# Kernel tuning notes

Measured on AMD Instinct MI355X. Metric: run time of the kernel, lower is better.

The kernel has to match this reference:

```python
import jax, jax.numpy as jnp
import numpy as np

EPS = 1e-5
B, N = 16, 131072

def _bn(x, g, b, m, v):
    # x: [C, N]; inference-mode batchnorm with given stats
    return g[:, None] * (x - m[:, None]) * jax.lax.rsqrt(v[:, None] + EPS) + b[:, None]

def _make_npts():
    base = N // B
    offs = np.linspace(-2048, 2048, B).astype(np.int64)
    npts = np.full(B, base, dtype=np.int64) + offs
    npts[-1] += N - npts.sum()
    assert npts.sum() == N and (npts > 0).all()
    return npts

def setup_inputs() -> dict:
    key = jax.random.key(0)
    ks = jax.random.split(key, 16)
    d = {}
    d["x"] = jax.random.normal(ks[0], (3, N), jnp.float32)
    d["npts"] = jnp.asarray(_make_npts(), jnp.int32)
    def w(k, o, i):
        return jax.random.normal(k, (o, i), jnp.float32) * (1.0 / np.sqrt(i))
    def bnp(k, c):
        k1, k2, k3, k4 = jax.random.split(k, 4)
        return (1.0 + 0.1 * jax.random.normal(k1, (c,), jnp.float32),
                0.1 * jax.random.normal(k2, (c,), jnp.float32),
                0.1 * jax.random.normal(k3, (c,), jnp.float32),
                0.5 + jax.random.uniform(k4, (c,), jnp.float32))
    d["W1"] = w(ks[1], 128, 3);   d["b1"] = jnp.zeros(128, jnp.float32)
    d["g1"], d["be1"], d["m1"], d["v1"] = bnp(ks[2], 128)
    d["W2"] = w(ks[3], 256, 128); d["b2"] = jnp.zeros(256, jnp.float32)
    d["g2"], d["be2"], d["m2"], d["v2"] = bnp(ks[4], 256)
    d["W3"] = w(ks[5], 512, 512); d["b3"] = jnp.zeros(512, jnp.float32)
    d["g3"], d["be3"], d["m3"], d["v3"] = bnp(ks[6], 512)
    d["W4"] = w(ks[7], 1024, 512); d["b4"] = jnp.zeros(1024, jnp.float32)
    d["g4"], d["be4"], d["m4"], d["v4"] = bnp(ks[8], 1024)
    return d

def reference(x, npts,
              W1, b1, g1, be1, m1, v1,
              W2, b2, g2, be2, m2, v2,
              W3, b3, g3, be3, m3, v3,
              W4, b4, g4, be4, m4, v4):
    # segment ids for the ragged point->cloud mapping (replaces torch.split loops)
    seg = jnp.repeat(jnp.arange(B, dtype=jnp.int32), npts, total_repeat_length=N)  # [N]
    h = jax.nn.relu(_bn(W1 @ x + b1[:, None], g1, be1, m1, v1))        # [128, N]
    f = _bn(W2 @ h + b2[:, None], g2, be2, m2, v2)                      # [256, N]
    g = jax.ops.segment_max(f.T, seg, num_segments=B)                   # [B, 256]
    gs = g[seg].T                                                       # [256, N] broadcast back
    xc = jnp.concatenate([gs, f], axis=0)                               # [512, N]
    h3 = jax.nn.relu(_bn(W3 @ xc + b3[:, None], g3, be3, m3, v3))       # [512, N]
    h4 = _bn(W4 @ h3 + b4[:, None], g4, be4, m4, v4)                    # [1024, N]
    v = jax.ops.segment_max(h4.T, seg, num_segments=B)                  # [B, 1024]
    return v
```

## Files before the change

### kernel.cpp

```cpp
#include <hip/hip_runtime.h>
#include <hip/hip_bf16.h>
#include <stdint.h>

#define NTOT 131072
#define NSEG 16
#define EPSV 1e-5f

typedef __attribute__((ext_vector_type(8))) short bf16x8;
typedef __attribute__((ext_vector_type(4))) float f32x4;

struct Args {
  const float* x; const int* npts;
  const float *W1,*b1,*g1,*be1,*m1,*v1;
  const float *W2,*b2,*g2,*be2,*m2,*v2;
  const float *W3,*b3,*g3,*be3,*m3,*v3;
  const float *W4,*b4,*g4,*be4,*m4,*v4;
  int* offs;
  float *a1,*c1,*a2,*c2,*a3,*c3,*a4,*c4;
  unsigned int *gkeys,*vkeys;
  unsigned short *w2b;
  unsigned short *w3p;
  unsigned short *w4p;
  unsigned short *fbufp;
  unsigned short *h3p;
  float* cseg;
  float* out;
};

__device__ inline unsigned int f2key(float f){ unsigned u=__float_as_uint(f); return (u&0x80000000u)? ~u : (u|0x80000000u); }
__device__ inline float key2f(unsigned k){ unsigned u=(k&0x80000000u)? (k^0x80000000u) : ~k; return __uint_as_float(u); }
__device__ inline unsigned short f2bf(float f){ __hip_bfloat16 h=__float2bfloat16(f); return *(unsigned short*)&h; }

__device__ inline void gl16(const void* g, void* l){
  __builtin_amdgcn_global_load_lds((const __attribute__((address_space(1))) unsigned int*)g,
                                   (__attribute__((address_space(3))) unsigned int*)l, 16, 0, 0);
}

__global__ void k_setup(Args A){
  int tid = threadIdx.x;
  if (tid==0){ int s=0; A.offs[0]=0; for (int i=0;i<NSEG;i++){ s+=A.npts[i]; A.offs[i+1]=s; } }
  for (int c=tid;c<128;c+=256){ float a=A.g1[c]*rsqrtf(A.v1[c]+EPSV); A.a1[c]=a; A.c1[c]=A.be1[c]+a*(A.b1[c]-A.m1[c]); }
  for (int c=tid;c<256;c+=256){ float a=A.g2[c]*rsqrtf(A.v2[c]+EPSV); A.a2[c]=a; A.c2[c]=A.be2[c]+a*(A.b2[c]-A.m2[c]); }
  for (int c=tid;c<512;c+=256){ float a=A.g3[c]*rsqrtf(A.v3[c]+EPSV); A.a3[c]=a; A.c3[c]=A.be3[c]+a*(A.b3[c]-A.m3[c]); }
  for (int c=tid;c<1024;c+=256){ float a=A.g4[c]*rsqrtf(A.v4[c]+EPSV); A.a4[c]=a; A.c4[c]=A.be4[c]+a*(A.b4[c]-A.m4[c]); }
  for (int i=tid;i<NSEG*256;i+=256)  A.gkeys[i]=0u;
  for (int i=tid;i<NSEG*1024;i+=256) A.vkeys[i]=0u;
}

__global__ void k_conv(Args A){
  const int n1=256*128;
  const int n2=8*4*512*8;
  const int n3=16*4*1024*8;
  for (int i = blockIdx.x*256+threadIdx.x; i < n1+n2+n3; i += gridDim.x*256){
    if (i<n1) A.w2b[i]=f2bf(A.W2[i]);
    else if (i<n1+n2){
      int o=i-n1; int j=o&7, cout=(o>>3)&511, g=o>>12; int ks=g>>2, kg=g&3;
      A.w3p[o]=f2bf(A.W3[(size_t)cout*512 + 256 + ks*32+kg*8+j]);
    } else {
      int o=i-n1-n2; int j=o&7, cout=(o>>3)&1023, g=o>>13; int ks=g>>2, kg=g&3;
      A.w4p[o]=f2bf(A.W4[(size_t)cout*512 + ks*32+kg*8+j]);
    }
  }
}

__global__ __launch_bounds__(256) void k_l12(Args A){
  __shared__ float w1s[384], a1s[128], c1s[128], a2s[256], c2s[256];
  __shared__ float xs[3][64];
  __shared__ int offs_s[NSEG+1], segp[64];
  __shared__ unsigned short hs[16*64*8];
  int tid=threadIdx.x, pt0=blockIdx.x*64;
  for (int i=tid;i<384;i+=256) w1s[i]=A.W1[i];
  if (tid<128){ a1s[tid]=A.a1[tid]; c1s[tid]=A.c1[tid]; }
  a2s[tid]=A.a2[tid]; c2s[tid]=A.c2[tid];
  if (tid<=NSEG) offs_s[tid]=A.offs[tid];
  if (tid<64){ xs[0][tid]=A.x[pt0+tid]; xs[1][tid]=A.x[NTOT+pt0+tid]; xs[2][tid]=A.x[2*NTOT+pt0+tid]; }
  __syncthreads();
  if (tid<64){ int gp=pt0+tid, s=0; while (gp>=offs_s[s+1]) s++; segp[tid]=s; }
  for (int pair=tid; pair<1024; pair+=256){
    int pt=pair&63, kc=pair>>6;
    float x0=xs[0][pt], x1=xs[1][pt], x2=xs[2][pt];
    unsigned short us[8];
    #pragma unroll
    for (int j=0;j<8;j++){
      int cin=kc*8+j;
      float v = fmaf(w1s[cin*3],x0, fmaf(w1s[cin*3+1],x1, w1s[cin*3+2]*x2));
      v = fmaxf(fmaf(a1s[cin],v,c1s[cin]), 0.f);
      us[j]=f2bf(v);
    }
    uint4 pk;
    pk.x=(unsigned)us[0]|((unsigned)us[1]<<16); pk.y=(unsigned)us[2]|((unsigned)us[3]<<16);
    pk.z=(unsigned)us[4]|((unsigned)us[5]<<16); pk.w=(unsigned)us[6]|((unsigned)us[7]<<16);
    *(uint4*)(&hs[(kc*64+pt)*8]) = pk;
  }
  __syncthreads();
  int lane=tid&63, wv=tid>>6, quad=lane>>4, l16=lane&15;
  int m0=wv*64;
  f32x4 acc[4][4];
  for (int a=0;a<4;a++)
    for (int b=0;b<4;b++)
      acc[a][b]=(f32x4){0.f,0.f,0.f,0.f};
  #pragma unroll
  for (int ks=0; ks<4; ++ks){
    bf16x8 bfr[4];
    #pragma unroll
    for (int nt=0; nt<4; ++nt) bfr[nt]=*(bf16x8*)(&hs[((ks*4+quad)*64 + nt*16 + l16)*8]);
    #pragma unroll
    for (int mt=0; mt<4; ++mt){
      bf16x8 afr = *(const bf16x8*)(&A.w2b[(m0+mt*16+l16)*128 + ks*32 + quad*8]);
      #pragma unroll
      for (int nt=0; nt<4; ++nt)
        acc[mt][nt]=__builtin_amdgcn_mfma_f32_16x16x32_bf16(afr, bfr[nt], acc[mt][nt], 0,0,0);
    }
  }
  bool uni = (segp[0]==segp[63]); int seg0=segp[0];
  size_t tb = (size_t)blockIdx.x*16384;
  #pragma unroll
  for (int mt=0;mt<4;++mt){
    int cout0=m0+mt*16+quad*4;
    int kg=cout0>>3, sub=cout0&7;
    float fv[4][4];
    #pragma unroll
    for (int nt=0;nt<4;++nt)
      #pragma unroll
      for (int r=0;r<4;++r)
        fv[nt][r]=fmaf(a2s[cout0+r], acc[mt][nt][r], c2s[cout0+r]);
    #pragma unroll
    for (int nt=0;nt<4;++nt){
      int ptl=nt*16+l16;
      uint2 pk;
      pk.x=(unsigned)f2bf(fv[nt][0])|((unsigned)f2bf(fv[nt][1])<<16);
      pk.y=(unsigned)f2bf(fv[nt][2])|((unsigned)f2bf(fv[nt][3])<<16);
      *(uint2*)&A.fbufp[tb + (size_t)((kg*64+ptl)*8+sub)] = pk;
    }
    #pragma unroll
    for (int r=0;r<4;++r){
      if (uni){
        float mv=fmaxf(fmaxf(fv[0][r],fv[1][r]),fmaxf(fv[2][r],fv[3][r]));
        #pragma unroll
        for (int off=8;off>=1;off>>=1) mv=fmaxf(mv, __shfl_xor(mv,off));
        if (l16==0) atomicMax(&A.gkeys[seg0*256+cout0+r], f2key(mv));
      } else {
        #pragma unroll
        for (int nt=0;nt<4;++nt)
          atomicMax(&A.gkeys[segp[nt*16+l16]*256+cout0+r], f2key(fv[nt][r]));
      }
    }
  }
}

__global__ void k_cseg(Args A){
  int seg = blockIdx.x>>1; int cout = (blockIdx.x&1)*256 + threadIdx.x;
  __shared__ float gs[256];
  gs[threadIdx.x] = key2f(A.gkeys[seg*256+threadIdx.x]);
  __syncthreads();
  const float* wrow = A.W3 + (size_t)cout*512;
  float s=0.f;
  #pragma unroll 8
  for (int k=0;k<256;k++) s = fmaf(wrow[k], gs[k], s);
  A.cseg[seg*512+cout]=s;
}

__global__ __launch_bounds__(512,2) void k_l3(Args A){
  __shared__ unsigned short wlds[8*4*256*8];
  __shared__ int offs_s[NSEG+1];
  int bid=blockIdx.x; int xcd=bid&7; int j=bid>>3;
  int cgrp=j&1, ptgrp=xcd*64+(j>>1);
  int tid=threadIdx.x, lane=tid&63, wv=tid>>6, quad=lane>>4, l16=lane&15;
  int mq=wv&1, tq=wv>>1;
  for (int i=wv*16;i<wv*16+16;++i){
    int slice=i>>2, q=i&3;
    const char* src=(const char*)(A.w3p + (size_t)slice*4096 + cgrp*2048 + q*512);
    gl16(src + lane*16, (char*)wlds + slice*4096 + q*1024);
  }
  if (tid<=NSEG) offs_s[tid]=A.offs[tid];
  __syncthreads();
  int tg = ptgrp*4 + tq, pt0 = tg*64;
  int sBeg=0; while (pt0 >= offs_s[sBeg+1]) sBeg++;
  int sEnd=sBeg; while (pt0+63 >= offs_s[sEnd+1]) sEnd++;
  bool uni=(sBeg==sEnd);
  int segl[4];
  if (!uni){
    #pragma unroll
    for (int nt=0;nt<4;++nt){ int gp=pt0+nt*16+l16, s=sBeg; while (gp>=offs_s[s+1]) s++; segl[nt]=s; }
  }
  f32x4 acc[8][4];
  for (int a=0;a<8;a++)
    for (int b=0;b<4;b++)
      acc[a][b]=(f32x4){0.f,0.f,0.f,0.f};
  const unsigned short* bsrc = A.fbufp + (size_t)tg*16384;
  bf16x8 bb[2][4];
  #pragma unroll
  for (int nt=0;nt<4;++nt) bb[0][nt]=*(const bf16x8*)(bsrc + (size_t)((quad*64 + nt*16 + l16)*8));
  #pragma unroll
  for (int nt=0;nt<4;++nt) bb[1][nt]=*(const bf16x8*)(bsrc + (size_t)(((4+quad)*64 + nt*16 + l16)*8));
  #pragma unroll
  for (int ksl=0; ksl<8; ++ksl){
    bf16x8 afr[8];
    #pragma unroll
    for (int mt=0;mt<8;++mt) afr[mt]=*(bf16x8*)(&wlds[((ksl*4+quad)*256 + mq*128 + mt*16 + l16)*8]);
    #pragma unroll
    for (int mt=0;mt<8;++mt)
      #pragma unroll
      for (int nt=0;nt<4;++nt)
        acc[mt][nt]=__builtin_amdgcn_mfma_f32_16x16x32_bf16(afr[mt], bb[ksl&1][nt], acc[mt][nt], 0,0,0);
    if (ksl+2<8){
      #pragma unroll
      for (int nt=0;nt<4;++nt) bb[ksl&1][nt]=*(const bf16x8*)(bsrc + (size_t)((((ksl+2)*4+quad)*64 + nt*16 + l16)*8));
    }
  }
  #pragma unroll
  for (int mt=0;mt<8;++mt){
    int cout0=cgrp*256 + mq*128 + mt*16 + quad*4;
    int kg=cout0>>3, sub=cout0&7;
    float sa[4],sc[4],csr[4];
    #pragma unroll
    for (int r=0;r<4;++r){ sa[r]=A.a3[cout0+r]; sc[r]=A.c3[cout0+r]; }
    if (uni){
      #pragma unroll
      for (int r=0;r<4;++r) csr[r]=A.cseg[sBeg*512+cout0+r];
    }
    #pragma unroll
    for (int nt=0;nt<4;++nt){
      int ptl=nt*16+l16;
      unsigned short us[4];
      #pragma unroll
      for (int r=0;r<4;++r){
        float cv = uni? csr[r] : A.cseg[segl[nt]*512+cout0+r];
        float hv = fmaxf(fmaf(sa[r], acc[mt][nt][r]+cv, sc[r]), 0.f);
        us[r]=f2bf(hv);
      }
      uint2 pk;
      pk.x=(unsigned)us[0]|((unsigned)us[1]<<16);
      pk.y=(unsigned)us[2]|((unsigned)us[3]<<16);
      *(uint2*)&A.h3p[(size_t)tg*32768 + (size_t)((kg*64+ptl)*8+sub)] = pk;
    }
  }
}

__global__ __launch_bounds__(512,2) void k_l4(Args A){
  __shared__ unsigned short wlds[16*4*128*8];
  __shared__ int offs_s[NSEG+1];
  int bid=blockIdx.x; int xcd=bid&7; int j=bid>>3;
  int cgrp=j&7, ptgrp=xcd*32+(j>>3);
  int tid=threadIdx.x, lane=tid&63, wv=tid>>6, quad=lane>>4, l16=lane&15;
  for (int i=wv*16;i<wv*16+16;++i){
    int slice=i>>1, half=i&1;
    const char* src=(const char*)(A.w4p + (size_t)slice*8192 + cgrp*1024 + half*512);
    gl16(src + lane*16, (char*)wlds + slice*2048 + half*1024);
  }
  if (tid<=NSEG) offs_s[tid]=A.offs[tid];
  __syncthreads();
  int tg = ptgrp*8 + wv, pt0 = tg*64;
  int sBeg=0; while (pt0 >= offs_s[sBeg+1]) sBeg++;
  int sEnd=sBeg; while (pt0+63 >= offs_s[sEnd+1]) sEnd++;
  bool uni=(sBeg==sEnd);
  int segl[4];
  if (!uni){
    #pragma unroll
    for (int nt=0;nt<4;++nt){ int gp=pt0+nt*16+l16, s=sBeg; while (gp>=offs_s[s+1]) s++; segl[nt]=s; }
  }
  f32x4 acc[8][4];
  for (int a=0;a<8;a++)
    for (int b=0;b<4;b++)
      acc[a][b]=(f32x4){0.f,0.f,0.f,0.f};
  const unsigned short* bsrc = A.h3p + (size_t)tg*32768;
  bf16x8 bb[2][4];
  #pragma unroll
  for (int nt=0;nt<4;++nt) bb[0][nt]=*(const bf16x8*)(bsrc + (size_t)((quad*64 + nt*16 + l16)*8));
  #pragma unroll
  for (int nt=0;nt<4;++nt) bb[1][nt]=*(const bf16x8*)(bsrc + (size_t)(((4+quad)*64 + nt*16 + l16)*8));
  #pragma unroll
  for (int ksl=0; ksl<16; ++ksl){
    bf16x8 afr[8];
    #pragma unroll
    for (int mt=0;mt<8;++mt) afr[mt]=*(bf16x8*)(&wlds[((ksl*4+quad)*128 + mt*16 + l16)*8]);
    #pragma unroll
    for (int mt=0;mt<8;++mt)
      #pragma unroll
      for (int nt=0;nt<4;++nt)
        acc[mt][nt]=__builtin_amdgcn_mfma_f32_16x16x32_bf16(afr[mt], bb[ksl&1][nt], acc[mt][nt], 0,0,0);
    if (ksl+2<16){
      #pragma unroll
      for (int nt=0;nt<4;++nt) bb[ksl&1][nt]=*(const bf16x8*)(bsrc + (size_t)((((ksl+2)*4+quad)*64 + nt*16 + l16)*8));
    }
  }
  #pragma unroll
  for (int mt=0;mt<8;++mt){
    int cout0=cgrp*128 + mt*16 + quad*4;
    #pragma unroll
    for (int r=0;r<4;++r){
      int cout=cout0+r;
      float sa=A.a4[cout], sc=A.c4[cout];
      float mv=-3.4e38f;
      #pragma unroll
      for (int nt=0;nt<4;++nt){
        float fv=fmaf(sa, acc[mt][nt][r], sc);
        if (uni) mv=fmaxf(mv,fv);
        else atomicMax(&A.vkeys[segl[nt]*1024+cout], f2key(fv));
      }
      if (uni){
        #pragma unroll
        for (int off=8;off>=1;off>>=1) mv=fmaxf(mv, __shfl_xor(mv,off));
        if (l16==0) atomicMax(&A.vkeys[sBeg*1024+cout], f2key(mv));
      }
    }
  }
}

__global__ void k_final(Args A){
  int i=blockIdx.x*256+threadIdx.x;
  if (i<NSEG*1024) A.out[i]=key2f(A.vkeys[i]);
}

extern "C" void kernel_launch(void* const* d_in, const int* in_sizes, int n_in,
                              void* d_out, int out_size, void* d_ws, size_t ws_size,
                              hipStream_t stream){
  Args A;
  A.x  =(const float*)d_in[0];  A.npts=(const int*)d_in[1];
  A.W1 =(const float*)d_in[2];  A.b1 =(const float*)d_in[3];
  A.g1 =(const float*)d_in[4];  A.be1=(const float*)d_in[5];
  A.m1 =(const float*)d_in[6];  A.v1 =(const float*)d_in[7];
  A.W2 =(const float*)d_in[8];  A.b2 =(const float*)d_in[9];
  A.g2 =(const float*)d_in[10]; A.be2=(const float*)d_in[11];
  A.m2 =(const float*)d_in[12]; A.v2 =(const float*)d_in[13];
  A.W3 =(const float*)d_in[14]; A.b3 =(const float*)d_in[15];
  A.g3 =(const float*)d_in[16]; A.be3=(const float*)d_in[17];
  A.m3 =(const float*)d_in[18]; A.v3 =(const float*)d_in[19];
  A.W4 =(const float*)d_in[20]; A.b4 =(const float*)d_in[21];
  A.g4 =(const float*)d_in[22]; A.be4=(const float*)d_in[23];
  A.m4 =(const float*)d_in[24]; A.v4 =(const float*)d_in[25];

  char* w=(char*)d_ws;
  auto alloc=[&](size_t b)->void*{ void* p=(void*)w; w += (b+255)&~(size_t)255; return p; };
  A.offs =(int*)alloc((NSEG+1)*4);
  A.a1=(float*)alloc(128*4);  A.c1=(float*)alloc(128*4);
  A.a2=(float*)alloc(256*4);  A.c2=(float*)alloc(256*4);
  A.a3=(float*)alloc(512*4);  A.c3=(float*)alloc(512*4);
  A.a4=(float*)alloc(1024*4); A.c4=(float*)alloc(1024*4);
  A.gkeys=(unsigned int*)alloc(NSEG*256*4);
  A.vkeys=(unsigned int*)alloc(NSEG*1024*4);
  A.cseg =(float*)alloc(NSEG*512*4);
  A.w2b=(unsigned short*)alloc(256*128*2);
  A.w3p=(unsigned short*)alloc(131072*2);
  A.w4p=(unsigned short*)alloc(524288*2);
  A.fbufp=(unsigned short*)alloc((size_t)2048*16384*2);
  A.h3p  =(unsigned short*)alloc((size_t)2048*32768*2);
  A.out=(float*)d_out;

  k_setup<<<dim3(1),dim3(256),0,stream>>>(A);
  k_conv <<<dim3(2688),dim3(256),0,stream>>>(A);
  k_l12  <<<dim3(NTOT/64),dim3(256),0,stream>>>(A);
  k_cseg <<<dim3(32),dim3(256),0,stream>>>(A);
  k_l3   <<<dim3(1024),dim3(512),0,stream>>>(A);
  k_l4   <<<dim3(2048),dim3(512),0,stream>>>(A);
  k_final<<<dim3(64),dim3(256),0,stream>>>(A);
}
```

Before: 683.8 us.

## Halve LDS weight footprint in L3/L4 GEMMs and raise occupancy to four blocks

The L3 and L4 MFMA kernels now stage the weight tile into LDS in two halves instead of all at once. This halves the shared-memory allocation per block, and launch bounds are raised from 2 to 4 blocks per CU to allow more concurrent waves. The second half is loaded between two block barriers, which adds a serialized reload with no overlap. The tighter register budget implied by the new launch bound may also force spills of the large accumulator array.

Result: slower. 2.115 ms (+209.3%).

```diff
diff --git a/kernel.cpp b/kernel.cpp
--- a/kernel.cpp
+++ b/kernel.cpp
@@ -160,18 +160,22 @@
   A.cseg[seg*512+cout]=s;
 }
 
-__global__ __launch_bounds__(512,2) void k_l3(Args A){
-  __shared__ unsigned short wlds[8*4*256*8];
+__global__ __launch_bounds__(512,4) void k_l3(Args A){
+  __shared__ unsigned short wlds[16*2048];
   __shared__ int offs_s[NSEG+1];
   int bid=blockIdx.x; int xcd=bid&7; int j=bid>>3;
   int cgrp=j&1, ptgrp=xcd*64+(j>>1);
   int tid=threadIdx.x, lane=tid&63, wv=tid>>6, quad=lane>>4, l16=lane&15;
   int mq=wv&1, tq=wv>>1;
-  for (int i=wv*16;i<wv*16+16;++i){
-    int slice=i>>2, q=i&3;
-    const char* src=(const char*)(A.w3p + (size_t)slice*4096 + cgrp*2048 + q*512);
-    gl16(src + lane*16, (char*)wlds + slice*4096 + q*1024);
-  }
+  auto stage=[&](int p){
+    #pragma unroll
+    for (int c=0;c<8;++c){
+      int i=wv*8+c; int sl=i>>2, q=i&3; int slice=p*16+sl;
+      const char* src=(const char*)(A.w3p + (size_t)slice*4096 + cgrp*2048 + q*512);
+      gl16(src + lane*16, (char*)wlds + sl*4096 + q*1024);
+    }
+  };
+  stage(0);
   if (tid<=NSEG) offs_s[tid]=A.offs[tid];
   __syncthreads();
   int tg = ptgrp*4 + tq, pt0 = tg*64;
@@ -193,19 +197,23 @@
   for (int nt=0;nt<4;++nt) bb[0][nt]=*(const bf16x8*)(bsrc + (size_t)((quad*64 + nt*16 + l16)*8));
   #pragma unroll
   for (int nt=0;nt<4;++nt) bb[1][nt]=*(const bf16x8*)(bsrc + (size_t)(((4+quad)*64 + nt*16 + l16)*8));
-  #pragma unroll
-  for (int ksl=0; ksl<8; ++ksl){
-    bf16x8 afr[8];
-    #pragma unroll
-    for (int mt=0;mt<8;++mt) afr[mt]=*(bf16x8*)(&wlds[((ksl*4+quad)*256 + mq*128 + mt*16 + l16)*8]);
-    #pragma unroll
-    for (int mt=0;mt<8;++mt)
-      #pragma unroll
-      for (int nt=0;nt<4;++nt)
-        acc[mt][nt]=__builtin_amdgcn_mfma_f32_16x16x32_bf16(afr[mt], bb[ksl&1][nt], acc[mt][nt], 0,0,0);
-    if (ksl+2<8){
-      #pragma unroll
-      for (int nt=0;nt<4;++nt) bb[ksl&1][nt]=*(const bf16x8*)(bsrc + (size_t)((((ksl+2)*4+quad)*64 + nt*16 + l16)*8));
+  for (int p=0;p<2;++p){
+    if (p){ __syncthreads(); stage(1); __syncthreads(); }
+    #pragma unroll
+    for (int kl=0; kl<4; ++kl){
+      int ksl=p*4+kl;
+      bf16x8 afr[8];
+      #pragma unroll
+      for (int mt=0;mt<8;++mt) afr[mt]=*(bf16x8*)(&wlds[((kl*4+quad)*256 + mq*128 + mt*16 + l16)*8]);
+      #pragma unroll
+      for (int mt=0;mt<8;++mt)
+        #pragma unroll
+        for (int nt=0;nt<4;++nt)
+          acc[mt][nt]=__builtin_amdgcn_mfma_f32_16x16x32_bf16(afr[mt], bb[ksl&1][nt], acc[mt][nt], 0,0,0);
+      if (ksl+2<8){
+        #pragma unroll
+        for (int nt=0;nt<4;++nt) bb[ksl&1][nt]=*(const bf16x8*)(bsrc + (size_t)((((ksl+2)*4+quad)*64 + nt*16 + l16)*8));
+      }
     }
   }
   #pragma unroll
@@ -237,17 +245,21 @@
   }
 }
 
-__global__ __launch_bounds__(512,2) void k_l4(Args A){
-  __shared__ unsigned short wlds[16*4*128*8];
+__global__ __launch_bounds__(512,4) void k_l4(Args A){
+  __shared__ unsigned short wlds[32*1024];
   __shared__ int offs_s[NSEG+1];
   int bid=blockIdx.x; int xcd=bid&7; int j=bid>>3;
   int cgrp=j&7, ptgrp=xcd*32+(j>>3);
   int tid=threadIdx.x, lane=tid&63, wv=tid>>6, quad=lane>>4, l16=lane&15;
-  for (int i=wv*16;i<wv*16+16;++i){
-    int slice=i>>1, half=i&1;
-    const char* src=(const char*)(A.w4p + (size_t)slice*8192 + cgrp*1024 + half*512);
-    gl16(src + lane*16, (char*)wlds + slice*2048 + half*1024);
-  }
+  auto stage=[&](int p){
+    #pragma unroll
+    for (int c=0;c<8;++c){
+      int i=wv*8+c; int sl=i>>1, half=i&1; int slice=p*32+sl;
+      const char* src=(const char*)(A.w4p + (size_t)slice*8192 + cgrp*1024 + half*512);
+      gl16(src + lane*16, (char*)wlds + sl*2048 + half*1024);
+    }
+  };
+  stage(0);
   if (tid<=NSEG) offs_s[tid]=A.offs[tid];
   __syncthreads();
   int tg = ptgrp*8 + wv, pt0 = tg*64;
@@ -269,19 +281,23 @@
   for (int nt=0;nt<4;++nt) bb[0][nt]=*(const bf16x8*)(bsrc + (size_t)((quad*64 + nt*16 + l16)*8));
   #pragma unroll
   for (int nt=0;nt<4;++nt) bb[1][nt]=*(const bf16x8*)(bsrc + (size_t)(((4+quad)*64 + nt*16 + l16)*8));
-  #pragma unroll
-  for (int ksl=0; ksl<16; ++ksl){
-    bf16x8 afr[8];
-    #pragma unroll
-    for (int mt=0;mt<8;++mt) afr[mt]=*(bf16x8*)(&wlds[((ksl*4+quad)*128 + mt*16 + l16)*8]);
-    #pragma unroll
-    for (int mt=0;mt<8;++mt)
-      #pragma unroll
-      for (int nt=0;nt<4;++nt)
-        acc[mt][nt]=__builtin_amdgcn_mfma_f32_16x16x32_bf16(afr[mt], bb[ksl&1][nt], acc[mt][nt], 0,0,0);
-    if (ksl+2<16){
-      #pragma unroll
-      for (int nt=0;nt<4;++nt) bb[ksl&1][nt]=*(const bf16x8*)(bsrc + (size_t)((((ksl+2)*4+quad)*64 + nt*16 + l16)*8));
+  for (int p=0;p<2;++p){
+    if (p){ __syncthreads(); stage(1); __syncthreads(); }
+    #pragma unroll
+    for (int kl=0; kl<8; ++kl){
+      int ksl=p*8+kl;
+      bf16x8 afr[8];
+      #pragma unroll
+      for (int mt=0;mt<8;++mt) afr[mt]=*(bf16x8*)(&wlds[((kl*4+quad)*128 + mt*16 + l16)*8]);
+      #pragma unroll
+      for (int mt=0;mt<8;++mt)
+        #pragma unroll
+        for (int nt=0;nt<4;++nt)
+          acc[mt][nt]=__builtin_amdgcn_mfma_f32_16x16x32_bf16(afr[mt], bb[ksl&1][nt], acc[mt][nt], 0,0,0);
+      if (ksl+2<16){
+        #pragma unroll
+        for (int nt=0;nt<4;++nt) bb[ksl&1][nt]=*(const bf16x8*)(bsrc + (size_t)((((ksl+2)*4+quad)*64 + nt*16 + l16)*8));
+      }
     }
   }
   #pragma unroll
```

## Stage activation tile in LDS and stream weights from global in layers 3 and 4

Applied to the files above, without the earlier changes.

Layers 3 and 4 previously staged a weight slice in shared memory per block and streamed activations from global per wave. Now each block handles one 64-point tile, loads that tile's activations into shared memory once, and each wave covers a distinct output-channel slice whose weight fragments are double-buffered from global/L2. The intent is to cut the activation re-reads across channel-group blocks and the per-block weight staging. In exchange, weight traffic now goes through L2 for every block and the grid for layer 3 doubles.

After: 973.9 us. 1.42x slower.

```diff
diff --git a/kernel.cpp b/kernel.cpp
--- a/kernel.cpp
+++ b/kernel.cpp
@@ -161,20 +161,17 @@
 }
 
 __global__ __launch_bounds__(512,2) void k_l3(Args A){
-  __shared__ unsigned short wlds[8*4*256*8];
+  __shared__ unsigned short xb[32*64*8];
   __shared__ int offs_s[NSEG+1];
-  int bid=blockIdx.x; int xcd=bid&7; int j=bid>>3;
-  int cgrp=j&1, ptgrp=xcd*64+(j>>1);
   int tid=threadIdx.x, lane=tid&63, wv=tid>>6, quad=lane>>4, l16=lane&15;
-  int mq=wv&1, tq=wv>>1;
-  for (int i=wv*16;i<wv*16+16;++i){
-    int slice=i>>2, q=i&3;
-    const char* src=(const char*)(A.w3p + (size_t)slice*4096 + cgrp*2048 + q*512);
-    gl16(src + lane*16, (char*)wlds + slice*4096 + q*1024);
+  int tg=blockIdx.x, pt0=tg*64;
+  {
+    const char* src=(const char*)(A.fbufp + (size_t)tg*16384);
+    #pragma unroll
+    for (int c=0;c<4;++c) gl16(src + (wv*4+c)*1024 + lane*16, (char*)xb + (wv*4+c)*1024);
   }
   if (tid<=NSEG) offs_s[tid]=A.offs[tid];
   __syncthreads();
-  int tg = ptgrp*4 + tq, pt0 = tg*64;
   int sBeg=0; while (pt0 >= offs_s[sBeg+1]) sBeg++;
   int sEnd=sBeg; while (pt0+63 >= offs_s[sEnd+1]) sEnd++;
   bool uni=(sBeg==sEnd);
@@ -183,34 +180,34 @@
     #pragma unroll
     for (int nt=0;nt<4;++nt){ int gp=pt0+nt*16+l16, s=sBeg; while (gp>=offs_s[s+1]) s++; segl[nt]=s; }
   }
-  f32x4 acc[8][4];
-  for (int a=0;a<8;a++)
+  int crow=wv*64;
+  bf16x8 af[2][4];
+  #pragma unroll
+  for (int mt=0;mt<4;++mt) af[0][mt]=*(const bf16x8*)(&A.w3p[((size_t)(0*4+quad)*512 + crow+mt*16+l16)*8]);
+  #pragma unroll
+  for (int mt=0;mt<4;++mt) af[1][mt]=*(const bf16x8*)(&A.w3p[((size_t)(1*4+quad)*512 + crow+mt*16+l16)*8]);
+  f32x4 acc[4][4];
+  for (int a=0;a<4;a++)
     for (int b=0;b<4;b++)
       acc[a][b]=(f32x4){0.f,0.f,0.f,0.f};
-  const unsigned short* bsrc = A.fbufp + (size_t)tg*16384;
-  bf16x8 bb[2][4];
-  #pragma unroll
-  for (int nt=0;nt<4;++nt) bb[0][nt]=*(const bf16x8*)(bsrc + (size_t)((quad*64 + nt*16 + l16)*8));
-  #pragma unroll
-  for (int nt=0;nt<4;++nt) bb[1][nt]=*(const bf16x8*)(bsrc + (size_t)(((4+quad)*64 + nt*16 + l16)*8));
   #pragma unroll
   for (int ksl=0; ksl<8; ++ksl){
-    bf16x8 afr[8];
-    #pragma unroll
-    for (int mt=0;mt<8;++mt) afr[mt]=*(bf16x8*)(&wlds[((ksl*4+quad)*256 + mq*128 + mt*16 + l16)*8]);
-    #pragma unroll
-    for (int mt=0;mt<8;++mt)
+    bf16x8 bfr[4];
+    #pragma unroll
+    for (int nt=0; nt<4; ++nt) bfr[nt]=*(bf16x8*)(&xb[((ksl*4+quad)*64 + nt*16 + l16)*8]);
+    #pragma unroll
+    for (int mt=0;mt<4;++mt)
       #pragma unroll
       for (int nt=0;nt<4;++nt)
-        acc[mt][nt]=__builtin_amdgcn_mfma_f32_16x16x32_bf16(afr[mt], bb[ksl&1][nt], acc[mt][nt], 0,0,0);
+        acc[mt][nt]=__builtin_amdgcn_mfma_f32_16x16x32_bf16(af[ksl&1][mt], bfr[nt], acc[mt][nt], 0,0,0);
     if (ksl+2<8){
       #pragma unroll
-      for (int nt=0;nt<4;++nt) bb[ksl&1][nt]=*(const bf16x8*)(bsrc + (size_t)((((ksl+2)*4+quad)*64 + nt*16 + l16)*8));
-    }
-  }
-  #pragma unroll
-  for (int mt=0;mt<8;++mt){
-    int cout0=cgrp*256 + mq*128 + mt*16 + quad*4;
+      for (int mt=0;mt<4;++mt) af[ksl&1][mt]=*(const bf16x8*)(&A.w3p[((size_t)((ksl+2)*4+quad)*512 + crow+mt*16+l16)*8]);
+    }
+  }
+  #pragma unroll
+  for (int mt=0;mt<4;++mt){
+    int cout0=crow + mt*16 + quad*4;
     int kg=cout0>>3, sub=cout0&7;
     float sa[4],sc[4],csr[4];
     #pragma unroll
@@ -238,19 +235,17 @@
 }
 
 __global__ __launch_bounds__(512,2) void k_l4(Args A){
-  __shared__ unsigned short wlds[16*4*128*8];
+  __shared__ unsigned short xb[64*64*8];
   __shared__ int offs_s[NSEG+1];
-  int bid=blockIdx.x; int xcd=bid&7; int j=bid>>3;
-  int cgrp=j&7, ptgrp=xcd*32+(j>>3);
   int tid=threadIdx.x, lane=tid&63, wv=tid>>6, quad=lane>>4, l16=lane&15;
-  for (int i=wv*16;i<wv*16+16;++i){
-    int slice=i>>1, half=i&1;
-    const char* src=(const char*)(A.w4p + (size_t)slice*8192 + cgrp*1024 + half*512);
-    gl16(src + lane*16, (char*)wlds + slice*2048 + half*1024);
+  int tg=blockIdx.x, pt0=tg*64;
+  {
+    const char* src=(const char*)(A.h3p + (size_t)tg*32768);
+    #pragma unroll
+    for (int c=0;c<8;++c) gl16(src + (wv*8+c)*1024 + lane*16, (char*)xb + (wv*8+c)*1024);
   }
   if (tid<=NSEG) offs_s[tid]=A.offs[tid];
   __syncthreads();
-  int tg = ptgrp*8 + wv, pt0 = tg*64;
   int sBeg=0; while (pt0 >= offs_s[sBeg+1]) sBeg++;
   int sEnd=sBeg; while (pt0+63 >= offs_s[sEnd+1]) sEnd++;
   bool uni=(sBeg==sEnd);
@@ -259,34 +254,34 @@
     #pragma unroll
     for (int nt=0;nt<4;++nt){ int gp=pt0+nt*16+l16, s=sBeg; while (gp>=offs_s[s+1]) s++; segl[nt]=s; }
   }
+  int crow=wv*128;
+  bf16x8 af[2][8];
+  #pragma unroll
+  for (int mt=0;mt<8;++mt) af[0][mt]=*(const bf16x8*)(&A.w4p[((size_t)(0*4+quad)*1024 + crow+mt*16+l16)*8]);
+  #pragma unroll
+  for (int mt=0;mt<8;++mt) af[1][mt]=*(const bf16x8*)(&A.w4p[((size_t)(1*4+quad)*1024 + crow+mt*16+l16)*8]);
   f32x4 acc[8][4];
   for (int a=0;a<8;a++)
     for (int b=0;b<4;b++)
       acc[a][b]=(f32x4){0.f,0.f,0.f,0.f};
-  const unsigned short* bsrc = A.h3p + (size_t)tg*32768;
-  bf16x8 bb[2][4];
-  #pragma unroll
-  for (int nt=0;nt<4;++nt) bb[0][nt]=*(const bf16x8*)(bsrc + (size_t)((quad*64 + nt*16 + l16)*8));
-  #pragma unroll
-  for (int nt=0;nt<4;++nt) bb[1][nt]=*(const bf16x8*)(bsrc + (size_t)(((4+quad)*64 + nt*16 + l16)*8));
   #pragma unroll
   for (int ksl=0; ksl<16; ++ksl){
-    bf16x8 afr[8];
-    #pragma unroll
-    for (int mt=0;mt<8;++mt) afr[mt]=*(bf16x8*)(&wlds[((ksl*4+quad)*128 + mt*16 + l16)*8]);
+    bf16x8 bfr[4];
+    #pragma unroll
+    for (int nt=0; nt<4; ++nt) bfr[nt]=*(bf16x8*)(&xb[((ksl*4+quad)*64 + nt*16 + l16)*8]);
     #pragma unroll
     for (int mt=0;mt<8;++mt)
       #pragma unroll
       for (int nt=0;nt<4;++nt)
-        acc[mt][nt]=__builtin_amdgcn_mfma_f32_16x16x32_bf16(afr[mt], bb[ksl&1][nt], acc[mt][nt], 0,0,0);
+        acc[mt][nt]=__builtin_amdgcn_mfma_f32_16x16x32_bf16(af[ksl&1][mt], bfr[nt], acc[mt][nt], 0,0,0);
     if (ksl+2<16){
       #pragma unroll
-      for (int nt=0;nt<4;++nt) bb[ksl&1][nt]=*(const bf16x8*)(bsrc + (size_t)((((ksl+2)*4+quad)*64 + nt*16 + l16)*8));
+      for (int mt=0;mt<8;++mt) af[ksl&1][mt]=*(const bf16x8*)(&A.w4p[((size_t)((ksl+2)*4+quad)*1024 + crow+mt*16+l16)*8]);
     }
   }
   #pragma unroll
   for (int mt=0;mt<8;++mt){
-    int cout0=cgrp*128 + mt*16 + quad*4;
+    int cout0=crow + mt*16 + quad*4;
     #pragma unroll
     for (int r=0;r<4;++r){
       int cout=cout0+r;
@@ -351,7 +346,7 @@
   k_conv <<<dim3(2688),dim3(256),0,stream>>>(A);
   k_l12  <<<dim3(NTOT/64),dim3(256),0,stream>>>(A);
   k_cseg <<<dim3(32),dim3(256),0,stream>>>(A);
-  k_l3   <<<dim3(1024),dim3(512),0,stream>>>(A);
+  k_l3   <<<dim3(2048),dim3(512),0,stream>>>(A);
   k_l4   <<<dim3(2048),dim3(512),0,stream>>>(A);
   k_final<<<dim3(64),dim3(256),0,stream>>>(A);
 }
```
